# Optimization experiments

Measured on AMD Instinct MI355X. Metric: run time of the kernel, lower is better.

Reference implementation:

```python
import jax, jax.numpy as jnp
from jax import lax
import numpy as np

B, T = 16, 64
NC, CS, HID, FEAT, ADIM = 32, 32, 128, 256, 6
CAT = NC * CS  # 1024


def _conv(x, w, b):
    # kernel 4, stride 2, padding 1 (NCHW / OIHW)
    y = lax.conv_general_dilated(x, w, window_strides=(2, 2), padding=[(1, 1), (1, 1)],
                                 dimension_numbers=('NCHW', 'OIHW', 'NCHW'))
    return y + b[None, :, None, None]


def _ln(x, g, b, eps=1e-5):
    # nn.LayerNorm([C,H,W]) normalizes over the last 3 dims with full affine
    m = jnp.mean(x, axis=(1, 2, 3), keepdims=True)
    v = jnp.var(x, axis=(1, 2, 3), keepdims=True)
    return (x - m) * lax.rsqrt(v + eps) * g[None] + b[None]


def setup_inputs() -> dict:
    key = jax.random.key(0)
    ks = jax.random.split(key, 12)
    w = lambda k, s: jax.random.normal(k, s, jnp.float32) * 0.02
    d = {
        'states': jax.random.normal(ks[0], (B, T, 3, 64, 64), jnp.float32),
        'actions': jax.random.normal(ks[1], (B, T, ADIM), jnp.float32),
        'conv1_w': w(ks[2], (32, 3, 4, 4)), 'conv1_b': jnp.zeros((32,), jnp.float32),
        'ln1_g': jnp.ones((32, 32, 32), jnp.float32), 'ln1_b': jnp.zeros((32, 32, 32), jnp.float32),
        'conv2_w': w(ks[3], (64, 32, 4, 4)), 'conv2_b': jnp.zeros((64,), jnp.float32),
        'ln2_g': jnp.ones((64, 16, 16), jnp.float32), 'ln2_b': jnp.zeros((64, 16, 16), jnp.float32),
        'conv3_w': w(ks[4], (128, 64, 4, 4)), 'conv3_b': jnp.zeros((128,), jnp.float32),
        'ln3_g': jnp.ones((128, 8, 8), jnp.float32), 'ln3_b': jnp.zeros((128, 8, 8), jnp.float32),
        'conv4_w': w(ks[5], (256, 128, 4, 4)), 'conv4_b': jnp.zeros((256,), jnp.float32),
        'ln4_g': jnp.ones((256, 4, 4), jnp.float32), 'ln4_b': jnp.zeros((256, 4, 4), jnp.float32),
        'fc_w': w(ks[6], (FEAT, 256 * 4 * 4)), 'fc_b': jnp.zeros((FEAT,), jnp.float32),
        'gru_wih': w(ks[7], (3 * HID, CAT + ADIM)), 'gru_whh': w(ks[8], (3 * HID, HID)),
        'gru_bih': jnp.zeros((3 * HID,), jnp.float32), 'gru_bhh': jnp.zeros((3 * HID,), jnp.float32),
        'prior_w': w(ks[9], (CAT, HID)), 'prior_b': jnp.zeros((CAT,), jnp.float32),
        'post_w': w(ks[10], (CAT, HID + FEAT)), 'post_b': jnp.zeros((CAT,), jnp.float32),
    }
    return d


def reference(states, actions, conv1_w, conv1_b, ln1_g, ln1_b, conv2_w, conv2_b, ln2_g, ln2_b,
              conv3_w, conv3_b, ln3_g, ln3_b, conv4_w, conv4_b, ln4_g, ln4_b, fc_w, fc_b,
              gru_wih, gru_whh, gru_bih, gru_bhh, prior_w, prior_b, post_w, post_b):
    bt = B * T
    # Encoder has no recurrent dependency -> batch all frames at once.
    x = states.reshape(bt, 3, 64, 64)
    x = jax.nn.silu(_ln(_conv(x, conv1_w, conv1_b), ln1_g, ln1_b))
    x = jax.nn.silu(_ln(_conv(x, conv2_w, conv2_b), ln2_g, ln2_b))
    x = jax.nn.silu(_ln(_conv(x, conv3_w, conv3_b), ln3_g, ln3_b))
    x = jax.nn.silu(_ln(_conv(x, conv4_w, conv4_b), ln4_g, ln4_b))
    feats = x.reshape(bt, -1) @ fc_w.T + fc_b              # [B*T, FEAT]
    feats = feats.reshape(B, T, FEAT).transpose(1, 0, 2)    # [T, B, FEAT]
    acts = actions.transpose(1, 0, 2)                       # [T, B, A]

    def step(carry, inp):
        h, z = carry
        a, f = inp
        xg = jnp.concatenate([z, a], axis=-1)
        gi = xg @ gru_wih.T + gru_bih
        gh = h @ gru_whh.T + gru_bhh
        ir, iz, inn = jnp.split(gi, 3, axis=-1)
        hr, hz, hn = jnp.split(gh, 3, axis=-1)
        r = jax.nn.sigmoid(ir + hr)
        u = jax.nn.sigmoid(iz + hz)
        n = jnp.tanh(inn + r * hn)
        h_new = (1.0 - u) * n + u * h                      # PyTorch GRUCell update
        prior = (h_new @ prior_w.T + prior_b).reshape(B, NC, CS)
        post = (jnp.concatenate([h_new, f], axis=-1) @ post_w.T + post_b).reshape(B, NC, CS)
        # eval-mode sampling: one-hot argmax (deterministic)
        z_new = jax.nn.one_hot(jnp.argmax(post, axis=-1), CS, dtype=h_new.dtype).reshape(B, CAT)
        return (h_new, z_new), (prior, post, h_new, z_new)

    init = (jnp.zeros((B, HID), states.dtype), jnp.zeros((B, CAT), states.dtype))
    _, (prior_l, post_l, h_seq, z_seq) = lax.scan(step, init, (acts, feats))
    return (prior_l.transpose(1, 0, 2, 3), post_l.transpose(1, 0, 2, 3),
            h_seq.transpose(1, 0, 2), z_seq.transpose(1, 0, 2))
```

## Files before the change

### kernel.cpp

```cpp
#include <hip/hip_runtime.h>
#include <math.h>


__device__ __forceinline__ float silu_f(float t){ return t / (1.f + __expf(-t)); }
__device__ __forceinline__ float sigm_f(float x){ return 1.f / (1.f + expf(-x)); }

__device__ __forceinline__ void block_stats_256(float s, float s2, int m,
                                                float& mean, float& rstd)
{
    __shared__ float red[8];
#pragma unroll
    for (int off = 32; off > 0; off >>= 1) {
        s  += __shfl_down(s, off);
        s2 += __shfl_down(s2, off);
    }
    int wv = threadIdx.x >> 6;
    if ((threadIdx.x & 63) == 0) { red[wv] = s; red[4 + wv] = s2; }
    __syncthreads();
    if (threadIdx.x == 0) {
        float S  = (red[0] + red[1]) + (red[2] + red[3]);
        float S2 = (red[4] + red[5]) + (red[6] + red[7]);
        float mu = S / m;
        float var = S2 / m - mu * mu;
        red[0] = mu;
        red[1] = rsqrtf(var + 1e-5f);
    }
    __syncthreads();
    mean = red[0]; rstd = red[1];
}

__global__ __launch_bounds__(256) void ln_fuse_k(float* __restrict__ x,
    const float* __restrict__ g, const float* __restrict__ b, int m)
{
    int n = blockIdx.x;
    float* p = x + (size_t)n * m;
    float s = 0.f, s2 = 0.f;
    for (int i = threadIdx.x * 4; i < m; i += 1024) {
        float4 v = *(const float4*)(p + i);
        s  += (v.x + v.y) + (v.z + v.w);
        s2 += (v.x*v.x + v.y*v.y) + (v.z*v.z + v.w*v.w);
    }
    float mean, rstd;
    block_stats_256(s, s2, m, mean, rstd);
    for (int i = threadIdx.x * 4; i < m; i += 1024) {
        float4 v  = *(float4*)(p + i);
        float4 gv = *(const float4*)(g + i);
        float4 bv = *(const float4*)(b + i);
        v.x = silu_f((v.x - mean) * rstd * gv.x + bv.x);
        v.y = silu_f((v.y - mean) * rstd * gv.y + bv.y);
        v.z = silu_f((v.z - mean) * rstd * gv.z + bv.z);
        v.w = silu_f((v.w - mean) * rstd * gv.w + bv.w);
        *(float4*)(p + i) = v;
    }
}

__global__ __launch_bounds__(256) void conv1_k(const float* __restrict__ in,
    const float* __restrict__ w, const float* __restrict__ bias, float* __restrict__ out)
{
    int n  = blockIdx.x;
    int yq = blockIdx.y;
    int tx = threadIdx.x & 31;
    int ty = threadIdx.x >> 5;
    int y  = yq * 8 + ty;
    const float* ip = in + (size_t)n * 12288;

    float okf[16]; int offs[16];
#pragma unroll
    for (int ky = 0; ky < 4; ky++) {
        int yy = 2 * y - 1 + ky;
        bool yok = ((unsigned)yy < 64u);
#pragma unroll
        for (int kx = 0; kx < 4; kx++) {
            int xx = 2 * tx - 1 + kx;
            bool ok = yok && ((unsigned)xx < 64u);
            okf[ky*4+kx]  = ok ? 1.f : 0.f;
            offs[ky*4+kx] = ok ? yy * 64 + xx : 0;
        }
    }
    float iv[48];
#pragma unroll
    for (int c = 0; c < 3; c++)
#pragma unroll
        for (int q = 0; q < 16; q++)
            iv[c*16+q] = ip[c*4096 + offs[q]] * okf[q];

    float* op = out + (size_t)n * 32768 + y * 32 + tx;
#pragma unroll 4
    for (int oc = 0; oc < 32; oc++) {
        float acc = bias[oc];
        const float* wp = w + oc * 48;
#pragma unroll
        for (int q = 0; q < 48; q++) acc += iv[q] * wp[q];
        op[oc * 1024] = acc;
    }
}

__global__ __launch_bounds__(256) void conv2_r(const float* __restrict__ in,
    const float* __restrict__ w, const float* __restrict__ bias,
    const float* __restrict__ lg, const float* __restrict__ lb,
    float* __restrict__ out)
{
    __shared__ __align__(16) float lds[8208];
    int n  = blockIdx.x;
    int tid = threadIdx.x;
    int wv  = tid >> 6;
    int g   = wv >> 1;
    int s   = ((wv & 1) << 6) | (tid & 63);
    int x   = s & 15, y0 = s >> 4;
    const float* ip = in + (size_t)n * 32768;

    int offs[2][16];
#pragma unroll
    for (int p = 0; p < 2; p++) {
        int y = y0 + 8 * p;
#pragma unroll
        for (int ky = 0; ky < 4; ky++) {
            int yi = 2 * y - 1 + ky;
#pragma unroll
            for (int kx = 0; kx < 4; kx++) {
                int xi = 2 * x - 1 + kx;
                bool ok = ((unsigned)yi < 32u) && ((unsigned)xi < 32u);
                int rot = ((xi >> 2) + (yi & 7)) & 7;
                int foff = yi * 32 + rot * 4 + (xi & 3);
                offs[p][ky*4+kx] = ok ? (4 + foff) * 4 : 0;
            }
        }
    }
    if (tid < 16) lds[(tid >> 2) * 1028 + (tid & 3)] = 0.f;

    float acc0[32], acc1[32];
#pragma unroll
    for (int i = 0; i < 32; i++) { float bv = bias[g*32 + i]; acc0[i] = bv; acc1[i] = bv; }

#pragma unroll 1
    for (int ch = 0; ch < 8; ch++) {
        __syncthreads();
        {
            const float4* gs = (const float4*)(ip + (ch << 12));
#pragma unroll
            for (int k = 0; k < 4; k++) {
                int gid = tid + (k << 8);
                int cc = gid >> 8, r = (gid >> 3) & 31, s4 = gid & 7;
                int rs = (s4 + (r & 7)) & 7;
                *(float4*)&lds[cc*1028 + 4 + r*32 + rs*4] = gs[gid];
            }
            int oc = tid >> 2, i4 = tid & 3;
            const float* wg = w + (size_t)oc * 512 + (ch << 6) + i4 * 4;
#pragma unroll
            for (int cc = 0; cc < 4; cc++)
                *(float4*)&lds[4112 + cc*1024 + oc*16 + i4*4] =
                    *(const float4*)(wg + cc * 16);
        }
        __syncthreads();
#pragma unroll 1
        for (int cc = 0; cc < 4; cc++) {
            const char* cb = (const char*)lds + cc * 4112;
            float iv0[16], iv1[16];
#pragma unroll
            for (int q = 0; q < 16; q++) {
                iv0[q] = *(const float*)(cb + offs[0][q]);
                iv1[q] = *(const float*)(cb + offs[1][q]);
            }
            const float* wb = &lds[4112 + cc*1024 + g*512];
#pragma unroll
            for (int o = 0; o < 32; o++) {
                float wt[16];
                *(float4*)&wt[0]  = *(const float4*)(wb + o*16);
                *(float4*)&wt[4]  = *(const float4*)(wb + o*16 + 4);
                *(float4*)&wt[8]  = *(const float4*)(wb + o*16 + 8);
                *(float4*)&wt[12] = *(const float4*)(wb + o*16 + 12);
#pragma unroll
                for (int q = 0; q < 16; q++) {
                    acc0[o] = fmaf(iv0[q], wt[q], acc0[o]);
                    acc1[o] = fmaf(iv1[q], wt[q], acc1[o]);
                }
            }
        }
    }
    float s1 = 0.f, s2 = 0.f;
#pragma unroll
    for (int o = 0; o < 32; o++) {
        s1 += acc0[o] + acc1[o];
        s2 += acc0[o]*acc0[o] + acc1[o]*acc1[o];
    }
    float mean, rstd;
    block_stats_256(s1, s2, 16384, mean, rstd);

    float* op = out + (size_t)n * 16384;
#pragma unroll
    for (int o = 0; o < 32; o++) {
        int f0 = (g*32 + o) * 256 + y0*16 + x;
        int f1 = (g*32 + o) * 256 + (y0+8)*16 + x;
        op[f0] = silu_f((acc0[o] - mean) * rstd * lg[f0] + lb[f0]);
        op[f1] = silu_f((acc1[o] - mean) * rstd * lg[f1] + lb[f1]);
    }
}

__global__ __launch_bounds__(256) void conv3_r(const float* __restrict__ in,
    const float* __restrict__ w, const float* __restrict__ bias,
    const float* __restrict__ lg, const float* __restrict__ lb,
    float* __restrict__ out)
{
    __shared__ __align__(16) float lds[9232];
    int n   = blockIdx.x;
    int tid = threadIdx.x;
    int g   = tid >> 5;
    int slot= tid & 31;
    int x   = slot & 7, y0 = slot >> 3;

    int offs[2][16];
#pragma unroll
    for (int p = 0; p < 2; p++) {
        int y = y0 + 4 * p;
#pragma unroll
        for (int ky = 0; ky < 4; ky++) {
            int yi = 2 * y - 1 + ky;
#pragma unroll
            for (int kx = 0; kx < 4; kx++) {
                int xi = 2 * x - 1 + kx;
                bool ok = ((unsigned)yi < 16u) && ((unsigned)xi < 16u);
                int rot = ((xi >> 2) + (yi & 3)) & 3;
                int foff = yi * 16 + rot * 4 + (xi & 3);
                offs[p][ky*4+kx] = ok ? (4 + foff) * 4 : 0;
            }
        }
    }
    if (tid < 16) lds[(tid >> 2) * 260 + (tid & 3)] = 0.f;

    float acc0[16], acc1[16];
#pragma unroll
    for (int i = 0; i < 16; i++) { float bv = bias[g*16 + i]; acc0[i] = bv; acc1[i] = bv; }

    const float* ip = in + (size_t)n * 16384;
#pragma unroll 1
    for (int ch = 0; ch < 16; ch++) {
        __syncthreads();
        {
            const float4* gs = (const float4*)(ip + (ch << 10));
            int cc = tid >> 6, r = (tid >> 2) & 15, s4 = tid & 3;
            int rs = (s4 + (r & 3)) & 3;
            *(float4*)&lds[cc*260 + 4 + r*16 + rs*4] = gs[tid];
            int oc = tid >> 1, h = tid & 1;
            const float* wg = w + (size_t)oc * 1024 + (ch << 6) + h * 8;
#pragma unroll
            for (int c2 = 0; c2 < 4; c2++) {
                *(float4*)&lds[1040 + c2*2048 + oc*16 + h*8]     = *(const float4*)(wg + c2*16);
                *(float4*)&lds[1040 + c2*2048 + oc*16 + h*8 + 4] = *(const float4*)(wg + c2*16 + 4);
            }
        }
        __syncthreads();
#pragma unroll 1
        for (int cc = 0; cc < 4; cc++) {
            const char* cb = (const char*)lds + cc * 1040;
            float iv0[16], iv1[16];
#pragma unroll
            for (int q = 0; q < 16; q++) {
                iv0[q] = *(const float*)(cb + offs[0][q]);
                iv1[q] = *(const float*)(cb + offs[1][q]);
            }
            const float* wb = &lds[1040 + cc*2048 + g*256];
#pragma unroll
            for (int o = 0; o < 16; o++) {
                float wt[16];
                *(float4*)&wt[0]  = *(const float4*)(wb + o*16);
                *(float4*)&wt[4]  = *(const float4*)(wb + o*16 + 4);
                *(float4*)&wt[8]  = *(const float4*)(wb + o*16 + 8);
                *(float4*)&wt[12] = *(const float4*)(wb + o*16 + 12);
#pragma unroll
                for (int q = 0; q < 16; q++) {
                    acc0[o] = fmaf(iv0[q], wt[q], acc0[o]);
                    acc1[o] = fmaf(iv1[q], wt[q], acc1[o]);
                }
            }
        }
    }
    float s1 = 0.f, s2 = 0.f;
#pragma unroll
    for (int o = 0; o < 16; o++) {
        s1 += acc0[o] + acc1[o];
        s2 += acc0[o]*acc0[o] + acc1[o]*acc1[o];
    }
    float mean, rstd;
    block_stats_256(s1, s2, 8192, mean, rstd);

    float* op = out + (size_t)n * 8192;
#pragma unroll
    for (int o = 0; o < 16; o++) {
        int f0 = (g*16 + o) * 64 + slot;
        int f1 = (g*16 + o) * 64 + slot + 32;
        op[f0] = silu_f((acc0[o] - mean) * rstd * lg[f0] + lb[f0]);
        op[f1] = silu_f((acc1[o] - mean) * rstd * lg[f1] + lb[f1]);
    }
}

__global__ __launch_bounds__(256) void tr_c4_k(const float* __restrict__ w,
                                               float* __restrict__ wt)
{
    int gi = blockIdx.x * 256 + threadIdx.x;
    int q  = gi & 15;
    int t  = gi >> 4;
    int oc = t & 255;
    int c  = t >> 8;
    wt[gi] = w[(size_t)oc * 2048 + c * 16 + q];
}

__global__ __launch_bounds__(256) void conv4_f(const float* __restrict__ in,
    const float* __restrict__ wT, const float* __restrict__ bias,
    const float* __restrict__ g, const float* __restrict__ bet, float* __restrict__ out)
{
    int n  = blockIdx.x;
    int oc = threadIdx.x;
    const float* ip = in + (size_t)n * 8192;

    float acc[16];
#pragma unroll
    for (int s = 0; s < 16; s++) acc[s] = bias[oc];

#pragma unroll 2
    for (int c = 0; c < 128; c++) {
        const float* ic = ip + c * 64;
        const float4* wp = (const float4*)(wT + ((size_t)c * 256 + oc) * 16);
        float wf[16];
        *(float4*)&wf[0]  = wp[0];
        *(float4*)&wf[4]  = wp[1];
        *(float4*)&wf[8]  = wp[2];
        *(float4*)&wf[12] = wp[3];
#pragma unroll
        for (int y = 0; y < 4; y++)
#pragma unroll
        for (int x = 0; x < 4; x++) {
            float a = acc[y * 4 + x];
#pragma unroll
            for (int ky = 0; ky < 4; ky++) {
                int yy = 2 * y - 1 + ky;
                if (yy < 0 || yy > 7) continue;
#pragma unroll
                for (int kx = 0; kx < 4; kx++) {
                    int xx = 2 * x - 1 + kx;
                    if (xx < 0 || xx > 7) continue;
                    a += wf[ky * 4 + kx] * ic[yy * 8 + xx];
                }
            }
            acc[y * 4 + x] = a;
        }
    }
    float s = 0.f, s2 = 0.f;
#pragma unroll
    for (int q = 0; q < 16; q++) { s += acc[q]; s2 += acc[q] * acc[q]; }
    float mean, rstd;
    block_stats_256(s, s2, 4096, mean, rstd);

    float* op = out + (size_t)n * 4096;
#pragma unroll
    for (int q = 0; q < 16; q++) {
        int flat = oc * 16 + q;
        float v = (acc[q] - mean) * rstd * g[flat] + bet[flat];
        op[flat] = silu_f(v);
    }
}

__global__ __launch_bounds__(256) void trfc_k(const float* __restrict__ w,
                                              float* __restrict__ wt)
{
    __shared__ float t[32][33];
    int bk = blockIdx.x * 32;
    int bj = blockIdx.y * 32;
    int lx = threadIdx.x & 31, ly = threadIdx.x >> 5;
#pragma unroll
    for (int s = 0; s < 4; s++)
        t[ly + 8*s][lx] = w[(size_t)(bj + ly + 8*s) * 4096 + bk + lx];
    __syncthreads();
#pragma unroll
    for (int s = 0; s < 4; s++)
        wt[(size_t)(bk + ly + 8*s) * 256 + bj + lx] = t[lx][ly + 8*s];
}

__global__ __launch_bounds__(256) void fc_k2(const float* __restrict__ a,
    const float* __restrict__ wT, const float* __restrict__ bias, float* __restrict__ o)
{
    int n0 = blockIdx.x * 8;
    int j  = threadIdx.x;
    float acc[8];
#pragma unroll
    for (int r = 0; r < 8; r++) acc[r] = 0.f;
    for (int k = 0; k < 4096; k += 4) {
        float wv0 = wT[(size_t)k * 256 + j];
        float wv1 = wT[(size_t)(k+1) * 256 + j];
        float wv2 = wT[(size_t)(k+2) * 256 + j];
        float wv3 = wT[(size_t)(k+3) * 256 + j];
#pragma unroll
        for (int r = 0; r < 8; r++) {
            const float* ar = a + (size_t)(n0 + r) * 4096 + k;
            acc[r] += wv0*ar[0] + wv1*ar[1] + wv2*ar[2] + wv3*ar[3];
        }
    }
    float bj = bias[j];
#pragma unroll
    for (int r = 0; r < 8; r++) o[(size_t)(n0 + r) * 256 + j] = acc[r] + bj;
}

__global__ __launch_bounds__(256) void fpost_k(const float* __restrict__ f,
    const float* __restrict__ w, const float* __restrict__ bias, float* __restrict__ o)
{
    int n0 = blockIdx.x * 4;
    int tid = threadIdx.x;
    float acc[4][4];
#pragma unroll
    for (int r = 0; r < 4; r++)
#pragma unroll
        for (int jj = 0; jj < 4; jj++) acc[r][jj] = 0.f;
    for (int k = 0; k < 256; k += 4) {
        float4 wv[4];
#pragma unroll
        for (int jj = 0; jj < 4; jj++)
            wv[jj] = *(const float4*)(w + (size_t)(tid + jj * 256) * 384 + 128 + k);
#pragma unroll
        for (int r = 0; r < 4; r++) {
            const float* fr = f + (size_t)(n0 + r) * 256 + k;
            float a0 = fr[0], a1 = fr[1], a2 = fr[2], a3 = fr[3];
#pragma unroll
            for (int jj = 0; jj < 4; jj++)
                acc[r][jj] += wv[jj].x*a0 + wv[jj].y*a1 + wv[jj].z*a2 + wv[jj].w*a3;
        }
    }
#pragma unroll
    for (int jj = 0; jj < 4; jj++) {
        float bj = bias[tid + jj * 256];
#pragma unroll
        for (int r = 0; r < 4; r++)
            o[(size_t)(n0 + r) * 1024 + tid + jj * 256] = acc[r][jj] + bj;
    }
}

__global__ __launch_bounds__(256) void prior_k(const float* __restrict__ h,
    const float* __restrict__ w, const float* __restrict__ bias, float* __restrict__ o)
{
    int n0 = blockIdx.x * 4;
    int tid = threadIdx.x;
    float acc[4][4];
#pragma unroll
    for (int r = 0; r < 4; r++)
#pragma unroll
        for (int jj = 0; jj < 4; jj++) acc[r][jj] = 0.f;
    for (int k = 0; k < 128; k += 4) {
        float4 wv[4];
#pragma unroll
        for (int jj = 0; jj < 4; jj++)
            wv[jj] = *(const float4*)(w + (size_t)(tid + jj * 256) * 128 + k);
#pragma unroll
        for (int r = 0; r < 4; r++) {
            const float* hr = h + (size_t)(n0 + r) * 128 + k;
            float a0 = hr[0], a1 = hr[1], a2 = hr[2], a3 = hr[3];
#pragma unroll
            for (int jj = 0; jj < 4; jj++)
                acc[r][jj] += wv[jj].x*a0 + wv[jj].y*a1 + wv[jj].z*a2 + wv[jj].w*a3;
        }
    }
#pragma unroll
    for (int jj = 0; jj < 4; jj++) {
        float bj = bias[tid + jj * 256];
#pragma unroll
        for (int r = 0; r < 4; r++)
            o[(size_t)(n0 + r) * 1024 + tid + jj * 256] = acc[r][jj] + bj;
    }
}

__global__ __launch_bounds__(128) void ai_k(const float* __restrict__ act,
    const float* __restrict__ wih, const float* __restrict__ bih, float* __restrict__ o)
{
    int n = blockIdx.x;
    int j = blockIdx.y * 128 + threadIdx.x;
    const float* ar = act + (size_t)n * 6;
    const float* wr = wih + (size_t)j * 1030 + 1024;
    float acc = bih[j];
#pragma unroll
    for (int k = 0; k < 6; k++) acc += ar[k] * wr[k];
    o[(size_t)n * 384 + j] = acc;
}

__global__ __launch_bounds__(256) void tr_k(const float* __restrict__ wih,
                                            float* __restrict__ wt)
{
    int g = blockIdx.x * 256 + threadIdx.x;
    int k = g / 384;
    int j = g - k * 384;
    wt[g] = wih[(size_t)j * 1030 + k];
}

__global__ __launch_bounds__(256) void tr_whh_k(const float* __restrict__ whh,
                                                float* __restrict__ wt)
{
    int g = blockIdx.x * 256 + threadIdx.x;
    int c  = g & 3;
    int jk = g >> 2;
    int j  = jk % 384;
    int k4 = jk / 384;
    wt[g] = whh[(size_t)j * 128 + k4 * 4 + c];
}

__global__ __launch_bounds__(256) void tr_pw_k(const float* __restrict__ pw,
                                               float* __restrict__ wt)
{
    int g = blockIdx.x * 256 + threadIdx.x;
    int c  = g & 3;
    int jk = g >> 2;
    int j  = jk & 1023;
    int k4 = jk >> 10;
    wt[g] = pw[(size_t)j * 384 + k4 * 4 + c];
}

__global__ __launch_bounds__(1024) void gru_k(const float* __restrict__ wihT,
    const float* __restrict__ whhV, const float* __restrict__ bhh,
    const float* __restrict__ ai, const float* __restrict__ fpost,
    const float* __restrict__ pwV, float* __restrict__ out,
    float* __restrict__ hs, float* __restrict__ ghs, int* __restrict__ idxs,
    int t0)
{
    float* out_post = out + 1048576;
    float* out_h    = out + 2097152;
    float* out_z    = out + 2228224;
    int b   = blockIdx.x;
    int tid = threadIdx.x;
    __shared__ __align__(16) float h[128];
    __shared__ float gi[384], gh[384];
    __shared__ int idx[32];
    if (t0 == 0) {
        if (tid < 128) h[tid] = 0.f;
        if (tid >= 512 && tid < 896) gh[tid - 512] = bhh[tid - 512];
    } else {
        if (tid < 128) h[tid] = hs[b * 128 + tid];
        if (tid >= 512 && tid < 896) gh[tid - 512] = ghs[b * 384 + tid - 512];
        if (tid < 32) idx[tid] = idxs[b * 32 + tid];
    }
    __syncthreads();

    const float4* h4  = (const float4*)h;
    const float4* wv4 = (const float4*)whhV;
    const float4* pv4 = (const float4*)pwV;

    for (int tt = 0; tt < 32; tt++) {
        int t = t0 + tt;
        int n = b * 64 + t;
        if (tid < 384) {
            float a = ai[(size_t)n * 384 + tid];
            if (t > 0) {
#pragma unroll 8
                for (int c = 0; c < 32; c++)
                    a += wihT[(size_t)(c * 32 + idx[c]) * 384 + tid];
            }
            gi[tid] = a;
        }
        __syncthreads();
        if (tid < 128) {
            float r  = sigm_f(gi[tid] + gh[tid]);
            float u  = sigm_f(gi[128 + tid] + gh[128 + tid]);
            float nn = tanhf(gi[256 + tid] + r * gh[256 + tid]);
            float hn = (1.f - u) * nn + u * h[tid];
            h[tid] = hn;
            out_h[(size_t)n * 128 + tid] = hn;
        }
        __syncthreads();
        if (tid < 512) {
            float a0 = fpost[(size_t)n * 1024 + tid];
            float a1 = fpost[(size_t)n * 1024 + 512 + tid];
#pragma unroll 16
            for (int k4 = 0; k4 < 32; k4++) {
                float4 hq = h4[k4];
                float4 w0 = pv4[k4 * 1024 + tid];
                float4 w1 = pv4[k4 * 1024 + 512 + tid];
                a0 += w0.x*hq.x + w0.y*hq.y + w0.z*hq.z + w0.w*hq.w;
                a1 += w1.x*hq.x + w1.y*hq.y + w1.z*hq.z + w1.w*hq.w;
            }
            out_post[(size_t)n * 1024 + tid]       = a0;
            out_post[(size_t)n * 1024 + 512 + tid] = a1;

            float b0 = a0, b1 = a1;
            int i0 = tid & 31, i1 = tid & 31;
#pragma unroll
            for (int m = 16; m >= 1; m >>= 1) {
                float ob0 = __shfl_xor(b0, m);
                int   oi0 = __shfl_xor(i0, m);
                float ob1 = __shfl_xor(b1, m);
                int   oi1 = __shfl_xor(i1, m);
                if (ob0 > b0 || (ob0 == b0 && oi0 < i0)) { b0 = ob0; i0 = oi0; }
                if (ob1 > b1 || (ob1 == b1 && oi1 < i1)) { b1 = ob1; i1 = oi1; }
            }
            out_z[(size_t)n * 1024 + tid]       = ((tid & 31) == i0) ? 1.f : 0.f;
            out_z[(size_t)n * 1024 + 512 + tid] = ((tid & 31) == i1) ? 1.f : 0.f;
            if ((tid & 31) == 0) {
                idx[tid >> 5]        = i0;
                idx[(tid >> 5) + 16] = i1;
            }
        } else if (tid < 896) {
            int r = tid - 512;
            float a2 = bhh[r];
#pragma unroll 8
            for (int k4 = 0; k4 < 32; k4++) {
                float4 wq = wv4[k4 * 384 + r];
                float4 hq = h4[k4];
                a2 += wq.x*hq.x + wq.y*hq.y + wq.z*hq.z + wq.w*hq.w;
            }
            gh[r] = a2;
        }
        __syncthreads();
    }
    if (t0 == 0) {
        if (tid < 128) hs[b * 128 + tid] = h[tid];
        else if (tid >= 512 && tid < 896) ghs[b * 384 + tid - 512] = gh[tid - 512];
        if (tid < 32) idxs[b * 32 + tid] = idx[tid];
    }
}

extern "C" void kernel_launch(void* const* d_in, const int* in_sizes, int n_in,
                              void* d_out, int out_size, void* d_ws, size_t ws_size,
                              hipStream_t stream)
{
    const float* states  = (const float*)d_in[0];
    const float* actions = (const float*)d_in[1];
    const float* c1w = (const float*)d_in[2];  const float* c1b = (const float*)d_in[3];
    const float* l1g = (const float*)d_in[4];  const float* l1b = (const float*)d_in[5];
    const float* c2w = (const float*)d_in[6];  const float* c2b = (const float*)d_in[7];
    const float* l2g = (const float*)d_in[8];  const float* l2b = (const float*)d_in[9];
    const float* c3w = (const float*)d_in[10]; const float* c3b = (const float*)d_in[11];
    const float* l3g = (const float*)d_in[12]; const float* l3b = (const float*)d_in[13];
    const float* c4w = (const float*)d_in[14]; const float* c4b = (const float*)d_in[15];
    const float* l4g = (const float*)d_in[16]; const float* l4b = (const float*)d_in[17];
    const float* fcw = (const float*)d_in[18]; const float* fcb = (const float*)d_in[19];
    const float* wih = (const float*)d_in[20]; const float* whh = (const float*)d_in[21];
    const float* bih = (const float*)d_in[22]; const float* bhh = (const float*)d_in[23];
    const float* prw = (const float*)d_in[24]; const float* prb = (const float*)d_in[25];
    const float* pw  = (const float*)d_in[26]; const float* pb  = (const float*)d_in[27];

    float* out = (float*)d_out;
    float* ws  = (float*)d_ws;

    size_t S = 64;
    {
        const size_t cands[4] = {1024, 512, 256, 128};
        for (int i = 0; i < 4; i++) {
            size_t need = (cands[i] * 49152ull + 3859968ull) * 4ull;
            if (need <= ws_size) { S = cands[i]; break; }
        }
    }
    int C = (int)(1024 / S);

    float* bufA  = ws;
    float* bufB  = bufA + S * 32768;
    float* feats = bufB + S * 16384;
    float* fpost = feats + 262144;
    float* aibuf = fpost + 1048576;
    float* wihT  = aibuf + 393216;
    float* fcwT  = wihT + 393216;
    float* whhV  = fcwT + 1048576;
    float* pwV   = whhV + 49152;
    float* c4wT  = pwV + 131072;
    float* hs    = c4wT + 524288;
    float* ghs   = hs + 2048;
    int*   idxs  = (int*)(ghs + 6144);

    trfc_k<<<dim3(128, 8), 256, 0, stream>>>(fcw, fcwT);
    tr_whh_k<<<192, 256, 0, stream>>>(whh, whhV);
    tr_pw_k<<<512, 256, 0, stream>>>(pw, pwV);
    tr_c4_k<<<2048, 256, 0, stream>>>(c4w, c4wT);

    for (int cc = 0; cc < C; cc++) {
        size_t n0 = (size_t)cc * S;
        conv1_k<<<dim3((unsigned)S, 4), 256, 0, stream>>>(states + n0 * 12288, c1w, c1b, bufA);
        ln_fuse_k<<<(unsigned)S, 256, 0, stream>>>(bufA, l1g, l1b, 32768);
        conv2_r<<<(unsigned)S, 256, 0, stream>>>(bufA, c2w, c2b, l2g, l2b, bufB);
        conv3_r<<<(unsigned)S, 256, 0, stream>>>(bufB, c3w, c3b, l3g, l3b, bufA);
        conv4_f<<<(unsigned)S, 256, 0, stream>>>(bufA, c4wT, c4b, l4g, l4b, bufB);
        fc_k2<<<(unsigned)(S / 8), 256, 0, stream>>>(bufB, fcwT, fcb, feats + n0 * 256);
    }

    fpost_k<<<256, 256, 0, stream>>>(feats, pw, pb, fpost);
    ai_k<<<dim3(1024, 3), 128, 0, stream>>>(actions, wih, bih, aibuf);
    tr_k<<<1536, 256, 0, stream>>>(wih, wihT);

    for (int t0 = 0; t0 < 64; t0 += 32)
        gru_k<<<16, 1024, 0, stream>>>(wihT, whhV, bhh, aibuf, fpost, pwV, out,
                                       hs, ghs, idxs, t0);
    prior_k<<<256, 256, 0, stream>>>(out + 2097152, prw, prb, out);
}
```

Baseline: 2.521 ms.

## Restructure conv3 to read wave-uniform weights from global via scalar loads

Conv3 now gives each wave 32 output channels and each lane one output pixel. Weights are read directly from global memory at wave-uniform addresses, which the compiler can turn into scalar loads, so they no longer need to be staged in LDS. The input tile is staged 16 channels at a time with a padded row stride of 17 to avoid bank conflicts, which cuts LDS use and the number of barriers. In exchange it relies on the scalar cache for weight bandwidth and holds 32 accumulators per thread instead of two 16-element sets.

```diff
diff --git a/kernel.cpp b/kernel.cpp
--- a/kernel.cpp
+++ b/kernel.cpp
@@ -201,95 +201,74 @@
     const float* __restrict__ lg, const float* __restrict__ lb,
     float* __restrict__ out)
 {
-    __shared__ __align__(16) float lds[9232];
+    __shared__ float lds[4416];
     int n   = blockIdx.x;
     int tid = threadIdx.x;
-    int g   = tid >> 5;
-    int slot= tid & 31;
-    int x   = slot & 7, y0 = slot >> 3;
-
-    int offs[2][16];
-#pragma unroll
-    for (int p = 0; p < 2; p++) {
-        int y = y0 + 4 * p;
-#pragma unroll
-        for (int ky = 0; ky < 4; ky++) {
-            int yi = 2 * y - 1 + ky;
-#pragma unroll
-            for (int kx = 0; kx < 4; kx++) {
-                int xi = 2 * x - 1 + kx;
-                bool ok = ((unsigned)yi < 16u) && ((unsigned)xi < 16u);
-                int rot = ((xi >> 2) + (yi & 3)) & 3;
-                int foff = yi * 16 + rot * 4 + (xi & 3);
-                offs[p][ky*4+kx] = ok ? (4 + foff) * 4 : 0;
-            }
-        }
-    }
-    if (tid < 16) lds[(tid >> 2) * 260 + (tid & 3)] = 0.f;
-
-    float acc0[16], acc1[16];
-#pragma unroll
-    for (int i = 0; i < 16; i++) { float bv = bias[g*16 + i]; acc0[i] = bv; acc1[i] = bv; }
+    int ocb = __builtin_amdgcn_readfirstlane((tid >> 6) << 5);
+    int s0  = tid & 63, y = s0 >> 3, x = s0 & 7;
+
+    int offs[16];
+#pragma unroll
+    for (int ky = 0; ky < 4; ky++) {
+        int yi = 2 * y - 1 + ky;
+#pragma unroll
+        for (int kx = 0; kx < 4; kx++) {
+            int xi = 2 * x - 1 + kx;
+            bool ok = ((unsigned)yi < 16u) && ((unsigned)xi < 16u);
+            offs[ky*4+kx] = ok ? (4 + yi * 17 + xi) : (tid & 3);
+        }
+    }
+    if (tid < 64) lds[(tid >> 2) * 276 + (tid & 3)] = 0.f;
+
+    float acc[32];
+#pragma unroll
+    for (int i = 0; i < 32; i++) acc[i] = bias[ocb + i];
 
     const float* ip = in + (size_t)n * 16384;
 #pragma unroll 1
-    for (int ch = 0; ch < 16; ch++) {
+    for (int ch = 0; ch < 4; ch++) {
         __syncthreads();
         {
-            const float4* gs = (const float4*)(ip + (ch << 10));
-            int cc = tid >> 6, r = (tid >> 2) & 15, s4 = tid & 3;
-            int rs = (s4 + (r & 3)) & 3;
-            *(float4*)&lds[cc*260 + 4 + r*16 + rs*4] = gs[tid];
-            int oc = tid >> 1, h = tid & 1;
-            const float* wg = w + (size_t)oc * 1024 + (ch << 6) + h * 8;
-#pragma unroll
-            for (int c2 = 0; c2 < 4; c2++) {
-                *(float4*)&lds[1040 + c2*2048 + oc*16 + h*8]     = *(const float4*)(wg + c2*16);
-                *(float4*)&lds[1040 + c2*2048 + oc*16 + h*8 + 4] = *(const float4*)(wg + c2*16 + 4);
+            const float4* gs = (const float4*)(ip + (ch << 12));
+#pragma unroll
+            for (int k = 0; k < 4; k++) {
+                int gid = tid + (k << 8);
+                int cc = gid >> 6, j = gid & 63;
+                int r = j >> 2, s4 = j & 3;
+                float4 v = gs[gid];
+                float* d = &lds[cc*276 + 4 + r*17 + s4*4];
+                d[0] = v.x; d[1] = v.y; d[2] = v.z; d[3] = v.w;
             }
         }
         __syncthreads();
 #pragma unroll 1
-        for (int cc = 0; cc < 4; cc++) {
-            const char* cb = (const char*)lds + cc * 1040;
-            float iv0[16], iv1[16];
-#pragma unroll
-            for (int q = 0; q < 16; q++) {
-                iv0[q] = *(const float*)(cb + offs[0][q]);
-                iv1[q] = *(const float*)(cb + offs[1][q]);
-            }
-            const float* wb = &lds[1040 + cc*2048 + g*256];
-#pragma unroll
-            for (int o = 0; o < 16; o++) {
-                float wt[16];
-                *(float4*)&wt[0]  = *(const float4*)(wb + o*16);
-                *(float4*)&wt[4]  = *(const float4*)(wb + o*16 + 4);
-                *(float4*)&wt[8]  = *(const float4*)(wb + o*16 + 8);
-                *(float4*)&wt[12] = *(const float4*)(wb + o*16 + 12);
-#pragma unroll
-                for (int q = 0; q < 16; q++) {
-                    acc0[o] = fmaf(iv0[q], wt[q], acc0[o]);
-                    acc1[o] = fmaf(iv1[q], wt[q], acc1[o]);
-                }
+        for (int cl = 0; cl < 16; cl++) {
+            int c = (ch << 4) + cl;
+            const float* cb = &lds[cl * 276];
+            float iv[16];
+#pragma unroll
+            for (int q = 0; q < 16; q++) iv[q] = cb[offs[q]];
+            const float* wp = w + ((size_t)ocb * 64 + c) * 16;
+#pragma unroll
+            for (int o = 0; o < 32; o++) {
+                const float* wo = wp + o * 1024;
+#pragma unroll
+                for (int q = 0; q < 16; q++)
+                    acc[o] = fmaf(iv[q], wo[q], acc[o]);
             }
         }
     }
     float s1 = 0.f, s2 = 0.f;
 #pragma unroll
-    for (int o = 0; o < 16; o++) {
-        s1 += acc0[o] + acc1[o];
-        s2 += acc0[o]*acc0[o] + acc1[o]*acc1[o];
-    }
+    for (int o = 0; o < 32; o++) { s1 += acc[o]; s2 += acc[o]*acc[o]; }
     float mean, rstd;
     block_stats_256(s1, s2, 8192, mean, rstd);
 
     float* op = out + (size_t)n * 8192;
 #pragma unroll
-    for (int o = 0; o < 16; o++) {
-        int f0 = (g*16 + o) * 64 + slot;
-        int f1 = (g*16 + o) * 64 + slot + 32;
-        op[f0] = silu_f((acc0[o] - mean) * rstd * lg[f0] + lb[f0]);
-        op[f1] = silu_f((acc1[o] - mean) * rstd * lg[f1] + lb[f1]);
+    for (int o = 0; o < 32; o++) {
+        int f0 = (ocb + o) * 64 + s0;
+        op[f0] = silu_f((acc[o] - mean) * rstd * lg[f0] + lb[f0]);
     }
 }
 
```

New measurement: 2.782 ms. 1.1x slower.
